# Optimization experiments

Measured on AMD Instinct MI355X. Metric: run time of the kernel, lower is better.

## Reference

```python
import jax, jax.numpy as jnp
import numpy as np

B, S, D = 2, 2048, 1024
H = 16
HD = D // H


def setup_inputs() -> dict:
    key = jax.random.key(0)
    k1, k2, k3 = jax.random.split(key, 3)
    x = jax.random.normal(k1, (B, S, D), dtype=jnp.float32)
    # xavier_uniform for qkv (fan_in=D, fan_out=3D) and out (D,D)
    lim_qkv = float(np.sqrt(6.0 / (D + 3 * D)))
    lim_out = float(np.sqrt(6.0 / (D + D)))
    W_qkv = jax.random.uniform(k2, (D, 3 * D), dtype=jnp.float32, minval=-lim_qkv, maxval=lim_qkv)
    b_qkv = jnp.zeros((3 * D,), dtype=jnp.float32)
    W_out = jax.random.uniform(k3, (D, D), dtype=jnp.float32, minval=-lim_out, maxval=lim_out)
    b_out = jnp.zeros((D,), dtype=jnp.float32)
    return {"x": x, "W_qkv": W_qkv, "b_qkv": b_qkv, "W_out": W_out, "b_out": b_out}


def reference(x, W_qkv, b_qkv, W_out, b_out):
    bs, seq_len, _ = x.shape
    qkv = x @ W_qkv + b_qkv                                  # [B,S,3D]
    qkv = qkv.reshape(bs, seq_len, H, 3 * HD).transpose(0, 2, 1, 3)  # [B,H,S,3HD]
    q, k, v = jnp.split(qkv, 3, axis=-1)                     # each [B,H,S,HD]
    score = jnp.einsum('bhqd,bhkd->bhqk', q, k) / jnp.sqrt(jnp.float32(HD))
    # Faithful to the torch code: mask float has -inf on strict upper triangle,
    # masked_fill treats nonzero (-inf) as True and fills with -9e-13 (~0),
    # so non-causal positions get logit -9e-13, NOT -inf.
    upper = jnp.triu(jnp.ones((seq_len, seq_len), dtype=bool), k=1)  # [S,S]
    score = jnp.where(upper, jnp.float32(-9e-13), score)
    score = jax.nn.softmax(score, axis=-1)
    value = jnp.einsum('bhqk,bhkd->bhqd', score, v)          # [B,H,S,HD]
    value = value.transpose(0, 2, 1, 3).reshape(bs, seq_len, D)
    out = value @ W_out + b_out                              # dropout p=0 (eval)
    return out
```

## Files before the change

### kernel.cpp

```cpp
#include <hip/hip_runtime.h>
#include <math.h>

#define B_ 2
#define S_ 2048
#define D_ 1024
#define H_ 16
#define HD_ 64

typedef unsigned short ushort8 __attribute__((ext_vector_type(8)));
typedef unsigned int u32x4 __attribute__((ext_vector_type(4)));
typedef _Float16 f16x8 __attribute__((ext_vector_type(8)));
typedef _Float16 f16x2 __attribute__((ext_vector_type(2)));
typedef float f32x4 __attribute__((ext_vector_type(4)));

__device__ __forceinline__ unsigned short f2h(float f) {
    union { _Float16 h; unsigned short u; } v;
    v.h = (_Float16)f;
    return v.u;
}
__device__ __forceinline__ float h2f(unsigned short u) {
    union { unsigned short u; _Float16 h; } v; v.u = u;
    return (float)v.h;
}
__device__ __forceinline__ ushort8 pack2x4h(f32x4 a, f32x4 b) {
    ushort8 hi;
    #pragma unroll
    for (int i = 0; i < 4; ++i) { hi[i] = f2h(a[i]); hi[4 + i] = f2h(b[i]); }
    return hi;
}

#define SWZ(row, col) ((((row)) << 6) + (((col)) ^ ((((row)) & 7) << 3)))

__device__ __forceinline__ f32x4 mfma16(f16x8 a, f16x8 b, f32x4 c) {
    return __builtin_amdgcn_mfma_f32_16x16x32_f16(a, b, c, 0, 0, 0);
}

typedef __attribute__((address_space(1))) const void gvoid_t;
typedef __attribute__((address_space(3))) void lvoid_t;
typedef __attribute__((address_space(3))) unsigned short lds_us_t;
__device__ __forceinline__ void gload_lds16(const void* g, void* l) {
    __builtin_amdgcn_global_load_lds((gvoid_t*)g, (lvoid_t*)l, 16, 0, 0);
}
__device__ __forceinline__ f16x8 dsr128(unsigned addr) {
    u32x4 r;
    asm volatile("ds_read_b128 %0, %1" : "=v"(r) : "v"(addr));
    union { u32x4 u; f16x8 h; } cv; cv.u = r; return cv.h;
}

#define EXPSC 0.18033688011f
#define EXP2R(x) __builtin_amdgcn_exp2f(x)

__global__ __launch_bounds__(256) void conv_rows_kernel(
    const float* __restrict__ in, unsigned short* __restrict__ ohi)
{
    const int id = blockIdx.x * 256 + threadIdx.x;
    const int r = id >> 7, c = id & 127;
    const float* s = in + (size_t)r * 1024 + c * 8;
    f32x4 v0 = *(const f32x4*)s, v1 = *(const f32x4*)(s + 4);
    ushort8 hi = pack2x4h(v0, v1);
    const int oc = (c & ~7) | ((c ^ r) & 7);
    *(ushort8*)&ohi[(size_t)r * 1024 + oc * 8] = hi;
}

__global__ __launch_bounds__(256) void conv_wt_kernel(
    const float* __restrict__ Wq, const float* __restrict__ Wo,
    unsigned short* __restrict__ Wqh, unsigned short* __restrict__ Woh)
{
    __shared__ float T[64][65];
    const float* W; int ldw, ny;
    unsigned short *oh;
    if (blockIdx.y < 48) { W = Wq; ldw = 3072; ny = blockIdx.y * 64; oh = Wqh; }
    else                 { W = Wo; ldw = 1024; ny = (blockIdx.y - 48) * 64; oh = Woh; }
    const int tid = threadIdx.x;
    const int kx = blockIdx.x * 64;
    const int kl = tid >> 2, c0 = (tid & 3) * 16;
    const float* s = W + (size_t)(kx + kl) * ldw + ny + c0;
    #pragma unroll
    for (int i = 0; i < 4; ++i) *(f32x4*)&T[kl][c0 + 4 * i] = *(const f32x4*)(s + 4 * i);
    __syncthreads();
    const int nl = tid >> 2, jj = (tid & 3) * 2;
    #pragma unroll
    for (int p = 0; p < 2; ++p) {
        const int j = jj + p;
        f32x4 a, b;
        #pragma unroll
        for (int i = 0; i < 4; ++i) a[i] = T[j * 8 + i][nl];
        #pragma unroll
        for (int i = 0; i < 4; ++i) b[i] = T[j * 8 + 4 + i][nl];
        ushort8 hi = pack2x4h(a, b);
        const int row = ny + nl;
        const int chunk = blockIdx.x * 8 + (j ^ (nl & 7));
        *(ushort8*)&oh[(size_t)row * 1024 + chunk * 8] = hi;
    }
}

template<int OUTMODE>
__global__ __launch_bounds__(256, 4) void gemm16_kernel(
    const unsigned short* __restrict__ Ah, const unsigned short* __restrict__ Bth,
    const float* __restrict__ bias, float* __restrict__ Cf, float* __restrict__ Cf1,
    unsigned short* __restrict__ Ohi,
    int M, int N, int K)
{
    __shared__ __align__(16) unsigned short lds[16384];

    const int tid = threadIdx.x, lane = tid & 63, w = tid >> 6;
    const int wm = w >> 1, wn = w & 1;
    const int gx = gridDim.x, nwg = gx * gridDim.y;
    const int lin = blockIdx.y * gx + blockIdx.x;
    const int nl = (lin & 7) * (nwg >> 3) + (lin >> 3);
    int mblk = nl / gx;
    int koff = 0;
    float* Cfw = Cf;
    bool dobias = (OUTMODE != 2);
    if (OUTMODE == 2) {
        const int halfrows = (int)(gridDim.y >> 1);
        if (mblk >= halfrows) { mblk -= halfrows; koff = 512; Cfw = Cf1; dobias = false; }
        else dobias = true;
    }
    const int m0 = mblk * 128, n0 = (nl % gx) * 128;
    const int col = lane & 15, g = lane >> 4;
    const int NT = K >> 5;

    const int sr0 = (w * 2 + 0) * 16 + (lane >> 2);
    const int sr1 = (w * 2 + 1) * 16 + (lane >> 2);
    const int scp = lane & 3;

    auto stage = [&](int tt) {
        unsigned short* dst = &lds[(tt & 1) * 8192];
        const int hi8 = (tt >> 1) * 8;
        const int tb4 = (tt & 1) << 2;
        #pragma unroll
        for (int q = 0; q < 2; ++q) {
            const int r = q ? sr1 : sr0;
            const int p = hi8 + ((tb4 ^ (r & 4)) | (scp ^ ((r >> 2) & 3)));
            const size_t go = (size_t)p * 8 + koff;
            const int slotb = (w * 2 + q) * 512;
            gload_lds16(Ah  + (size_t)(m0 + r) * 1024 + go, dst + 0    + slotb);
            gload_lds16(Bth + (size_t)(n0 + r) * 1024 + go, dst + 4096 + slotb);
        }
    };

    const unsigned ldsb = (unsigned)(size_t)(lds_us_t*)lds;
    const unsigned sk = (unsigned)(((g ^ (col & 3) ^ ((col >> 2) & 3)) & 3) << 4);
    const unsigned aB = ldsb + (unsigned)((wm * 64 + col) * 64) + sk;
    const unsigned bB = ldsb + 8192u + (unsigned)((wn * 64 + col) * 64) + sk;

    f32x4 acc[4][4] = {};

    stage(0);
    stage(1);

    for (int tt = 0; tt < NT; ++tt) {
        if (tt + 1 < NT) asm volatile("s_waitcnt vmcnt(4)" ::: "memory");
        else             asm volatile("s_waitcnt vmcnt(0)" ::: "memory");
        __builtin_amdgcn_s_barrier();
        __builtin_amdgcn_sched_barrier(0);
        const unsigned bo = (unsigned)((tt & 1) * 16384);

        f16x8 a[4], b[4];
        #pragma unroll
        for (int i = 0; i < 4; ++i) a[i] = dsr128(aB + bo + i * 1024u);
        #pragma unroll
        for (int i = 0; i < 4; ++i) b[i] = dsr128(bB + bo + i * 1024u);

        asm volatile("s_waitcnt lgkmcnt(0)" ::: "memory");
        __builtin_amdgcn_sched_barrier(0);
        __builtin_amdgcn_s_setprio(1);
        #pragma unroll
        for (int mi = 0; mi < 4; ++mi)
            #pragma unroll
            for (int nj = 0; nj < 4; ++nj)
                acc[mi][nj] = mfma16(a[mi], b[nj], acc[mi][nj]);
        __builtin_amdgcn_s_setprio(0);
        __builtin_amdgcn_s_barrier();
        __builtin_amdgcn_sched_barrier(0);
        if (tt + 2 < NT) stage(tt + 2);
    }

    __syncthreads();
    float* ow = (float*)((char*)lds + w * 8192);
    const int nc = (lane & 7) * 8;
    const int nabs = n0 + wn * 64 + nc;
    f32x4 bi0 = {}, bi1 = {};
    if (dobias) { bi0 = *(const f32x4*)&bias[nabs]; bi1 = *(const f32x4*)&bias[nabs + 4]; }
    #pragma unroll
    for (int half = 0; half < 2; ++half) {
        __builtin_amdgcn_wave_barrier();
        #pragma unroll
        for (int ml = 0; ml < 2; ++ml)
            #pragma unroll
            for (int nj = 0; nj < 4; ++nj)
                #pragma unroll
                for (int r = 0; r < 4; ++r)
                    ow[(ml * 16 + g * 4 + r) * 64 + nj * 16 + col] = acc[half * 2 + ml][nj][r];
        __builtin_amdgcn_wave_barrier();
        #pragma unroll
        for (int it = 0; it < 4; ++it) {
            const int rl = it * 8 + (lane >> 3);
            f32x4 v0 = *(const f32x4*)&ow[rl * 64 + nc];
            f32x4 v1 = *(const f32x4*)&ow[rl * 64 + nc + 4];
            if (dobias) { v0 += bi0; v1 += bi1; }
            const int m = m0 + wm * 64 + half * 32 + rl;
            if (OUTMODE == 1) {
                ushort8 hi = pack2x4h(v0, v1);
                const int chunk = (lane & 7) ^ (m & 7);
                *(ushort8*)&Ohi[(size_t)m * N + n0 + wn * 64 + chunk * 8] = hi;
            } else {
                *(f32x4*)&Cfw[(size_t)m * N + nabs] = v0;
                *(f32x4*)&Cfw[(size_t)m * N + nabs + 4] = v1;
            }
        }
        __builtin_amdgcn_wave_barrier();
    }
}

__global__ __launch_bounds__(256) void addp_kernel(
    float* __restrict__ out, const float* __restrict__ p1)
{
    const size_t idx = ((size_t)blockIdx.x * 256 + threadIdx.x) * 4;
    f32x4 v = *(const f32x4*)&out[idx];
    f32x4 u = *(const f32x4*)&p1[idx];
    v += u;
    *(f32x4*)&out[idx] = v;
}

__global__ __launch_bounds__(256) void vsuf_part_kernel(
    const unsigned short* __restrict__ qh, float* __restrict__ tsum)
{
    const int bh = blockIdx.x, tg = blockIdx.y;
    const int b = bh >> 4, h = bh & 15;
    const unsigned short* qhB = qh + (size_t)b * 2048 * 3072;
    const int tl = threadIdx.x >> 6, lane = threadIdx.x & 63;
    const int t = tg * 4 + tl;
    const int dgrp = lane & 7, rr = lane >> 3;
    const int colbase = h * 192 + 128;
    float sacc[8] = {};
    for (int kk = 0; kk < 8; ++kk) {
        const int row = t * 64 + rr + kk * 8;
        const size_t off = (size_t)row * 3072 + colbase + ((dgrp ^ rr) << 3);
        ushort8 vh = *(const ushort8*)&qhB[off];
        #pragma unroll
        for (int e = 0; e < 8; ++e) sacc[e] += h2f(vh[e]);
    }
    #pragma unroll
    for (int off = 8; off < 64; off <<= 1)
        #pragma unroll
        for (int e = 0; e < 8; ++e) sacc[e] += __shfl_xor(sacc[e], off);
    if (rr == 0) {
        float* dst = &tsum[((size_t)bh * 32 + t) * 64 + dgrp * 8];
        f32x4 v0, v1;
        #pragma unroll
        for (int e = 0; e < 4; ++e) { v0[e] = sacc[e]; v1[e] = sacc[4 + e]; }
        *(f32x4*)dst = v0;
        *(f32x4*)(dst + 4) = v1;
    }
}

__global__ __launch_bounds__(64) void vsuf_scan_kernel(
    const float* __restrict__ tsum, float* __restrict__ vsuf)
{
    const int bh = blockIdx.x, d = threadIdx.x;
    float acc = 0.f;
    vsuf[((size_t)bh * 33 + 32) * 64 + d] = 0.f;
    for (int t = 31; t >= 0; --t) {
        acc += tsum[((size_t)bh * 32 + t) * 64 + d];
        vsuf[((size_t)bh * 33 + t) * 64 + d] = acc;
    }
}

__global__ __launch_bounds__(256, 4) void attn_kernel(
    const unsigned short* __restrict__ qh,
    const float* __restrict__ vsuf,
    unsigned short* __restrict__ ohi,
    float* __restrict__ partO, float* __restrict__ partML)
{
    __shared__ __align__(16) unsigned short lds[16384];

    const int tid = threadIdx.x, lane = tid & 63, w = tid >> 6;
    const int g = lane >> 4, oct = g * 8, col = lane & 15;
    const int bh = blockIdx.y;
    const int b = bh >> 4, h = bh & 15;
    const unsigned short* qhB = qh + (size_t)b * 2048 * 3072;
    const float* vsufB = vsuf + (size_t)bh * 33 * 64;
    const int brow = b * 2048;
    const int kp = tid & 31, dg = tid >> 5;

    const int job = blockIdx.x;
    int i, s = 0, slot = -1;
    if (job < 32) { const int r = job; i = 16 + (r >> 1); s = r & 1; slot = (bh << 5) + r; }
    else { i = 47 - job; }
    const int q0 = i * 64;
    const int ntile_all = i + 1;
    const int t_begin = s * 16;
    const int t_end = (slot < 0) ? ntile_all : min(t_begin + 16, ntile_all);
    const bool isseg = (slot >= 0);

    auto kissue = [&](int ktbase, ushort8* kr) {
        #pragma unroll
        for (int j = 0; j < 2; ++j) {
            const int cc = w * 2 + j;
            const int row = ktbase + cc * 8 + (lane >> 3);
            kr[j] = *(const ushort8*)(qhB + (size_t)row * 3072 + h * 192 + 64 + (lane & 7) * 8);
        }
    };
    auto kwrite = [&](const ushort8* kr) {
        #pragma unroll
        for (int j = 0; j < 2; ++j) {
            const int cc = w * 2 + j;
            *(ushort8*)&lds[cc * 512 + lane * 8] = kr[j];
        }
    };
    auto vload = [&](int ktbase, f16x8& vA, f16x8& vB) {
        const int r0 = ktbase + 2 * kp, r1 = r0 + 1;
        const int pA = dg ^ (r0 & 7), pB = dg ^ (r1 & 7);
        vA = *(const f16x8*)&qhB[(size_t)r0 * 3072 + h * 192 + 128 + pA * 8];
        vB = *(const f16x8*)&qhB[(size_t)r1 * 3072 + h * 192 + 128 + pB * 8];
    };
    auto vwrite = [&](f16x8 vA, f16x8 vB) {
        #pragma unroll
        for (int e = 0; e < 8; ++e) {
            const int d = dg * 8 + e;
            f16x2 pr; pr[0] = vA[e]; pr[1] = vB[e];
            *(f16x2*)&lds[8192 + SWZ(d, 2 * kp)] = pr;
        }
    };

    #pragma unroll
    for (int j = 0; j < 2; ++j) {
        const int cc = w * 2 + j;
        const int row = q0 + cc * 8 + (lane >> 3);
        gload_lds16(qhB + (size_t)row * 3072 + h * 192 + (lane & 7) * 8,
                    &lds[cc * 512]);
    }
    ushort8 kr[2]; f16x8 vA, vB;
    kissue(t_begin * 64, kr);
    vload(t_begin * 64, vA, vB);
    __syncthreads();
    f16x8 qfh[2];
    {
        const int qrow = w * 16 + col;
        qfh[0] = *(const f16x8*)&lds[SWZ(qrow, oct)];
        qfh[1] = *(const f16x8*)&lds[SWZ(qrow, 32 + oct)];
    }
    __syncthreads();
    kwrite(kr);
    vwrite(vA, vB);
    __syncthreads();

    const int qg = q0 + w * 16 + col;
    float l_run = 0.f;
    f32x4 oacc[4] = {};

    for (int t = t_begin; t < t_end; ++t) {
        const int kt = t * 64;
        const bool pf = (t + 1 < t_end);
        if (pf) { kissue(kt + 64, kr); vload(kt + 64, vA, vB); }

        f32x4 sacc[4] = {};
        #pragma unroll
        for (int c = 0; c < 2; ++c)
            #pragma unroll
            for (int t4 = 0; t4 < 4; ++t4) {
                const int krow = t4 * 16 + col;
                f16x8 khf = *(const f16x8*)&lds[SWZ(krow, c * 32 + oct)];
                sacc[t4] = mfma16(khf, qfh[c], sacc[t4]);
            }

        unsigned short* Pw = &lds[12288 + w * 1024];
        if (t == ntile_all - 1) {
            #pragma unroll
            for (int t4 = 0; t4 < 4; ++t4)
                #pragma unroll
                for (int rp = 0; rp < 2; ++rp) {
                    const int k0 = kt + t4 * 16 + g * 4 + rp * 2;
                    float s0 = sacc[t4][rp * 2]     * EXPSC;
                    float s1 = sacc[t4][rp * 2 + 1] * EXPSC;
                    if (k0 > qg)     s0 = 0.0f;
                    if (k0 + 1 > qg) s1 = 0.0f;
                    float e0 = EXP2R(s0), e1 = EXP2R(s1);
                    l_run += e0 + e1;
                    f16x2 pk; pk[0] = (_Float16)e0; pk[1] = (_Float16)e1;
                    *(f16x2*)&Pw[SWZ(col, t4 * 16 + g * 4 + rp * 2)] = pk;
                }
        } else {
            #pragma unroll
            for (int t4 = 0; t4 < 4; ++t4)
                #pragma unroll
                for (int rp = 0; rp < 2; ++rp) {
                    float e0 = EXP2R(sacc[t4][rp * 2]     * EXPSC);
                    float e1 = EXP2R(sacc[t4][rp * 2 + 1] * EXPSC);
                    l_run += e0 + e1;
                    f16x2 pk; pk[0] = (_Float16)e0; pk[1] = (_Float16)e1;
                    *(f16x2*)&Pw[SWZ(col, t4 * 16 + g * 4 + rp * 2)] = pk;
                }
        }

        __builtin_amdgcn_wave_barrier();

        __syncthreads();
        if (pf) kwrite(kr);

        #pragma unroll
        for (int c = 0; c < 2; ++c) {
            f16x8 pfv = *(const f16x8*)&Pw[SWZ(col, c * 32 + oct)];
            #pragma unroll
            for (int dt = 0; dt < 4; ++dt) {
                f16x8 vh = *(const f16x8*)&lds[8192 + SWZ(dt * 16 + col, c * 32 + oct)];
                oacc[dt] = mfma16(vh, pfv, oacc[dt]);
            }
        }

        __syncthreads();
        if (pf) vwrite(vA, vB);
    }

    float lt = l_run;
    lt += __shfl_xor(lt, 16);
    lt += __shfl_xor(lt, 32);

    if (isseg) {
        float* po = partO + (size_t)slot * 4096;
        #pragma unroll
        for (int dt = 0; dt < 4; ++dt)
            #pragma unroll
            for (int r = 0; r < 4; ++r)
                po[(dt * 16 + g * 4 + r) * 64 + w * 16 + col] = oacc[dt][r];
        if (g == 0) partML[(size_t)slot * 128 + w * 16 + col] = lt;
        return;
    }

    lt += (float)(S_ - q0 - 64);
    {
        const float* vs = vsufB + (size_t)(i + 1) * 64;
        #pragma unroll
        for (int dt = 0; dt < 4; ++dt)
            #pragma unroll
            for (int r = 0; r < 4; ++r)
                oacc[dt][r] += vs[dt * 16 + g * 4 + r];
    }
    const float inv = 1.f / lt;
    float* ow = (float*)&lds[w * 4096];
    const int q = lane >> 2, jj = lane & 3;
    #pragma unroll
    for (int half = 0; half < 2; ++half) {
        __builtin_amdgcn_wave_barrier();
        #pragma unroll
        for (int t4 = 0; t4 < 2; ++t4)
            #pragma unroll
            for (int r = 0; r < 4; ++r)
                ow[col * 40 + t4 * 16 + g * 4 + r] = oacc[half * 2 + t4][r] * inv;
        __builtin_amdgcn_wave_barrier();
        f32x4 v0 = *(const f32x4*)&ow[q * 40 + jj * 8];
        f32x4 v1 = *(const f32x4*)&ow[q * 40 + jj * 8 + 4];
        ushort8 hi = pack2x4h(v0, v1);
        const int m = brow + q0 + w * 16 + q;
        const int chunk = (half * 4 + jj) ^ (m & 7);
        *(ushort8*)&ohi[(size_t)m * 1024 + h * 64 + chunk * 8] = hi;
    }
}

__global__ __launch_bounds__(256) void attn_combine_kernel(
    const float* __restrict__ partO, const float* __restrict__ partML,
    const float* __restrict__ vsuf,
    unsigned short* __restrict__ ohi)
{
    const int i = 16 + blockIdx.x;
    const int bh = blockIdx.y;
    const int b = bh >> 4, h = bh & 15;
    const float* vsufB = vsuf + (size_t)bh * 33 * 64;
    const int brow = b * 2048;
    const int nseg = 2;
    const int slot0 = (bh << 5) + (i - 16) * 2;
    const int q = threadIdx.x & 63, dgrp = threadIdx.x >> 6;
    const int q0 = i * 64;

    float lstar = (float)(S_ - q0 - 64);

    float od[16];
    const float* vs = vsufB + (size_t)(i + 1) * 64 + dgrp * 16;
    #pragma unroll
    for (int k = 0; k < 16; ++k) od[k] = vs[k];

    for (int sg = 0; sg < nseg; ++sg) {
        lstar += partML[(size_t)(slot0 + sg) * 128 + q];
        const float* po = partO + (size_t)(slot0 + sg) * 4096 + (size_t)(dgrp * 16) * 64 + q;
        #pragma unroll
        for (int k = 0; k < 16; ++k) od[k] += po[k * 64];
    }

    const float inv = 1.f / lstar;
    f32x4 a0, a1, b0, b1;
    #pragma unroll
    for (int k = 0; k < 4; ++k) {
        a0[k] = od[k] * inv; a1[k] = od[4 + k] * inv;
        b0[k] = od[8 + k] * inv; b1[k] = od[12 + k] * inv;
    }
    ushort8 hi0 = pack2x4h(a0, a1);
    ushort8 hi1 = pack2x4h(b0, b1);
    const int mrow = brow + q0 + q;
    const int c0 = (dgrp * 2) ^ (mrow & 7);
    const int c1 = (dgrp * 2 + 1) ^ (mrow & 7);
    const size_t base = (size_t)mrow * 1024 + h * 64;
    *(ushort8*)&ohi[base + c0 * 8] = hi0;
    *(ushort8*)&ohi[base + c1 * 8] = hi1;
}

extern "C" void kernel_launch(void* const* d_in, const int* in_sizes, int n_in,
                              void* d_out, int out_size, void* d_ws, size_t ws_size,
                              hipStream_t stream) {
    const float* x     = (const float*)d_in[0];
    const float* W_qkv = (const float*)d_in[1];
    const float* b_qkv = (const float*)d_in[2];
    const float* W_out = (const float*)d_in[3];
    const float* b_out = (const float*)d_in[4];
    float* out = (float*)d_out;

    unsigned short* us  = (unsigned short*)d_ws;
    unsigned short* Wqh = us;
    unsigned short* Woh = Wqh + (size_t)3072 * 1024;
    unsigned short* XAhi = Woh + (size_t)1024 * 1024;
    unsigned short* QKVh = XAhi + (size_t)4096 * 1024;
    float* tsum   = (float*)(QKVh + (size_t)4096 * 3072);
    float* vsuf   = tsum + (size_t)32 * 32 * 64;
    float* partML = vsuf + (size_t)32 * 33 * 64;

    float* partO = out;
    float* p1    = (float*)QKVh;

    conv_wt_kernel<<<dim3(16, 64), 256, 0, stream>>>(W_qkv, W_out, Wqh, Woh);
    conv_rows_kernel<<<dim3(2048), 256, 0, stream>>>(x, XAhi);

    gemm16_kernel<1><<<dim3(24, 32), 256, 0, stream>>>(
        XAhi, Wqh, b_qkv, nullptr, nullptr, QKVh, 4096, 3072, 1024);

    vsuf_part_kernel<<<dim3(32, 8), 256, 0, stream>>>(QKVh, tsum);
    vsuf_scan_kernel<<<dim3(32), 64, 0, stream>>>(tsum, vsuf);

    attn_kernel<<<dim3(48, 32), 256, 0, stream>>>(
        QKVh, vsuf, XAhi, partO, partML);
    attn_combine_kernel<<<dim3(16, 32), 256, 0, stream>>>(
        partO, partML, vsuf, XAhi);

    gemm16_kernel<2><<<dim3(8, 64), 256, 0, stream>>>(
        XAhi, Woh, b_out, out, p1, nullptr, 4096, 1024, 512);
    addp_kernel<<<dim3(4096), 256, 0, stream>>>(out, p1);
}
```

Measured before the change: 132.8 us.

## Double-buffer K/V tiles in LDS and load K directly to LDS

The attention loop's K and V tiles are now double-buffered in LDS, with the next tile written into the alternate buffer while the current one is consumed. This removes one of the two block-wide barriers per iteration. K is fetched with direct global-to-LDS loads instead of going through registers. LDS use per block grows from 32 KB to 40 KB, which may reduce occupancy at the requested 4 blocks per CU. The direct K load also relies on the single remaining barrier to order the async writes correctly.

```diff
diff --git a/kernel.cpp b/kernel.cpp
--- a/kernel.cpp
+++ b/kernel.cpp
@@ -274,7 +274,7 @@
     unsigned short* __restrict__ ohi,
     float* __restrict__ partO, float* __restrict__ partML)
 {
-    __shared__ __align__(16) unsigned short lds[16384];
+    __shared__ __align__(16) unsigned short lds[20480];
 
     const int tid = threadIdx.x, lane = tid & 63, w = tid >> 6;
     const int g = lane >> 4, oct = g * 8, col = lane & 15;
@@ -295,19 +295,13 @@
     const int t_end = (slot < 0) ? ntile_all : min(t_begin + 16, ntile_all);
     const bool isseg = (slot >= 0);
 
-    auto kissue = [&](int ktbase, ushort8* kr) {
+    auto gloadK = [&](int ktbase, unsigned kb) {
         #pragma unroll
         for (int j = 0; j < 2; ++j) {
             const int cc = w * 2 + j;
             const int row = ktbase + cc * 8 + (lane >> 3);
-            kr[j] = *(const ushort8*)(qhB + (size_t)row * 3072 + h * 192 + 64 + (lane & 7) * 8);
-        }
-    };
-    auto kwrite = [&](const ushort8* kr) {
-        #pragma unroll
-        for (int j = 0; j < 2; ++j) {
-            const int cc = w * 2 + j;
-            *(ushort8*)&lds[cc * 512 + lane * 8] = kr[j];
+            gload_lds16(qhB + (size_t)row * 3072 + h * 192 + 64 + (lane & 7) * 8,
+                        &lds[kb + cc * 512]);
         }
     };
     auto vload = [&](int ktbase, f16x8& vA, f16x8& vB) {
@@ -316,12 +310,12 @@
         vA = *(const f16x8*)&qhB[(size_t)r0 * 3072 + h * 192 + 128 + pA * 8];
         vB = *(const f16x8*)&qhB[(size_t)r1 * 3072 + h * 192 + 128 + pB * 8];
     };
-    auto vwrite = [&](f16x8 vA, f16x8 vB) {
+    auto vwrite = [&](f16x8 vA, f16x8 vB, unsigned vb) {
         #pragma unroll
         for (int e = 0; e < 8; ++e) {
             const int d = dg * 8 + e;
             f16x2 pr; pr[0] = vA[e]; pr[1] = vB[e];
-            *(f16x2*)&lds[8192 + SWZ(d, 2 * kp)] = pr;
+            *(f16x2*)&lds[vb + SWZ(d, 2 * kp)] = pr;
         }
     };
 
@@ -332,8 +326,7 @@
         gload_lds16(qhB + (size_t)row * 3072 + h * 192 + (lane & 7) * 8,
                     &lds[cc * 512]);
     }
-    ushort8 kr[2]; f16x8 vA, vB;
-    kissue(t_begin * 64, kr);
+    f16x8 vA, vB;
     vload(t_begin * 64, vA, vB);
     __syncthreads();
     f16x8 qfh[2];
@@ -343,18 +336,25 @@
         qfh[1] = *(const f16x8*)&lds[SWZ(qrow, 32 + oct)];
     }
     __syncthreads();
-    kwrite(kr);
-    vwrite(vA, vB);
+    gloadK(t_begin * 64, 0u);
+    vwrite(vA, vB, 8192u);
     __syncthreads();
 
     const int qg = q0 + w * 16 + col;
     float l_run = 0.f;
     f32x4 oacc[4] = {};
 
+    int cur = 0;
     for (int t = t_begin; t < t_end; ++t) {
         const int kt = t * 64;
         const bool pf = (t + 1 < t_end);
-        if (pf) { kissue(kt + 64, kr); vload(kt + 64, vA, vB); }
+        const unsigned kb  = (unsigned)(cur * 4096);
+        const unsigned vb  = 8192u + (unsigned)(cur * 4096);
+        const unsigned kbn = (unsigned)((cur ^ 1) * 4096);
+        const unsigned vbn = 8192u + (unsigned)((cur ^ 1) * 4096);
+
+        f16x8 vA2, vB2;
+        if (pf) { vload(kt + 64, vA2, vB2); gloadK(kt + 64, kbn); }
 
         f32x4 sacc[4] = {};
         #pragma unroll
@@ -362,11 +362,11 @@
             #pragma unroll
             for (int t4 = 0; t4 < 4; ++t4) {
                 const int krow = t4 * 16 + col;
-                f16x8 khf = *(const f16x8*)&lds[SWZ(krow, c * 32 + oct)];
+                f16x8 khf = *(const f16x8*)&lds[kb + SWZ(krow, c * 32 + oct)];
                 sacc[t4] = mfma16(khf, qfh[c], sacc[t4]);
             }
 
-        unsigned short* Pw = &lds[12288 + w * 1024];
+        unsigned short* Pw = &lds[16384 + w * 1024];
         if (t == ntile_all - 1) {
             #pragma unroll
             for (int t4 = 0; t4 < 4; ++t4)
@@ -395,23 +395,22 @@
                 }
         }
 
+        if (pf) vwrite(vA2, vB2, vbn);
+
         __builtin_amdgcn_wave_barrier();
-
-        __syncthreads();
-        if (pf) kwrite(kr);
 
         #pragma unroll
         for (int c = 0; c < 2; ++c) {
             f16x8 pfv = *(const f16x8*)&Pw[SWZ(col, c * 32 + oct)];
             #pragma unroll
             for (int dt = 0; dt < 4; ++dt) {
-                f16x8 vh = *(const f16x8*)&lds[8192 + SWZ(dt * 16 + col, c * 32 + oct)];
+                f16x8 vh = *(const f16x8*)&lds[vb + SWZ(dt * 16 + col, c * 32 + oct)];
                 oacc[dt] = mfma16(vh, pfv, oacc[dt]);
             }
         }
 
         __syncthreads();
-        if (pf) vwrite(vA, vB);
+        cur ^= 1;
     }
 
     float lt = l_run;
```

Result: no change. 133.2 us (+0.3%).
